# Kernel optimization log

Hardware: AMD Instinct MI355X
Metric: run time of the kernel (lower is better)

The kernel has to match this reference:

```python
import jax, jax.numpy as jnp
import numpy as np

N = 8192          # num_nodes
F_IN = 512        # num_features
D = 256           # embedding_dim
C = 40            # num_classes
E = 262144        # num_edges (avg degree 32)
ALPHA = 0.5
LN_EPS = 1e-5


def _layer_norm(x, eps=LN_EPS):
    # F.layer_norm over last dim, no affine params
    mu = jnp.mean(x, axis=-1, keepdims=True)
    var = jnp.var(x, axis=-1, keepdims=True)
    return (x - mu) * jax.lax.rsqrt(var + eps)


def setup_inputs() -> dict:
    key = jax.random.key(0)
    ks = jax.random.split(key, 16)
    s_in = 1.0 / np.sqrt(F_IN)
    s_d = 1.0 / np.sqrt(D)
    inp = {
        "X": jax.random.normal(ks[0], (N, F_IN), dtype=jnp.float32),
        "edge_row": jnp.sort(jax.random.randint(ks[1], (E,), 0, N)),
        "edge_col": jax.random.randint(ks[2], (E,), 0, N),
        "edge_weight": jax.random.uniform(ks[3], (E,), dtype=jnp.float32),
        # MLP embedding: Linear(F_IN, D)
        "W_emb": jax.random.uniform(ks[4], (F_IN, D), minval=-s_in, maxval=s_in),
        "b_emb": jax.random.uniform(ks[5], (D,), minval=-s_in, maxval=s_in),
        # attention projections: Linear(D, D) x3
        "W_q": jax.random.uniform(ks[6], (D, D), minval=-s_d, maxval=s_d),
        "b_q": jax.random.uniform(ks[7], (D,), minval=-s_d, maxval=s_d),
        "W_k": jax.random.uniform(ks[8], (D, D), minval=-s_d, maxval=s_d),
        "b_k": jax.random.uniform(ks[9], (D,), minval=-s_d, maxval=s_d),
        "W_v": jax.random.uniform(ks[10], (D, D), minval=-s_d, maxval=s_d),
        "b_v": jax.random.uniform(ks[11], (D,), minval=-s_d, maxval=s_d),
        # GNN linear: Linear(D, D)
        "W_gnn": jax.random.uniform(ks[12], (D, D), minval=-s_d, maxval=s_d),
        "b_gnn": jax.random.uniform(ks[13], (D,), minval=-s_d, maxval=s_d),
        # classifier: Linear(D, C)
        "W_cls": jax.random.uniform(ks[14], (D, C), minval=-s_d, maxval=s_d),
        "b_cls": jax.random.uniform(ks[15], (C,), minval=-s_d, maxval=s_d),
    }
    return inp


def reference(X, edge_row, edge_col, edge_weight,
              W_emb, b_emb, W_q, b_q, W_k, b_k, W_v, b_v,
              W_gnn, b_gnn, W_cls, b_cls):
    # embedding MLP
    Z0 = X @ W_emb + b_emb                      # [N, D]
    # global attention with QK layer-norm
    Q = _layer_norm(Z0 @ W_q + b_q)             # [N, D]
    K = _layer_norm(Z0 @ W_k + b_k)             # [N, D]
    V = Z0 @ W_v + b_v                          # [N, D]
    scores = Q @ K.T                            # [N, N]
    attn = jax.nn.softmax(scores, axis=-1)      # [N, N]
    Z_A = attn @ V                              # [N, D]
    # sparse GNN branch: spmm(A, linear(Z0))
    H = Z0 @ W_gnn + b_gnn                      # [N, D]
    msg = H[edge_col] * edge_weight[:, None]    # [E, D]
    gnn_out = jax.ops.segment_sum(msg, edge_row, num_segments=N)  # [N, D]
    # weighted blend + classifier
    Z_out = (1.0 - ALPHA) * Z_A + ALPHA * gnn_out
    Y_hat = Z_out @ W_cls + b_cls               # [N, C]
    return (Y_hat, attn)
```

## Files before the change

kernel.cpp:

```cpp
#include <hip/hip_runtime.h>
#include <hip/hip_bf16.h>

#define N_NODES 8192
#define F_IN    512
#define DIM     256
#define NCLS    40

typedef __attribute__((ext_vector_type(8))) short bf16x8;
typedef __attribute__((ext_vector_type(4))) float f32x4;

#define MFMA16 __builtin_amdgcn_mfma_f32_16x16x32_bf16

static __device__ __forceinline__ unsigned short f2bf(float x) {
    __hip_bfloat16 h = __float2bfloat16(x);
    return *reinterpret_cast<unsigned short*>(&h);
}
static __device__ __forceinline__ float bf2f(unsigned short u) {
    union { unsigned int u32; float f; } v; v.u32 = ((unsigned int)u) << 16;
    return v.f;
}
static __device__ __forceinline__ void gll16(const void* g, void* l) {
    __builtin_amdgcn_global_load_lds(
        (const __attribute__((address_space(1))) unsigned int*)g,
        (__attribute__((address_space(3))) unsigned int*)l, 16, 0, 0);
}

__global__ __launch_bounds__(256) void split_kernel(
    const float* __restrict__ X,
    unsigned short* __restrict__ Xh, unsigned short* __restrict__ Xl)
{
    const size_t i = ((size_t)blockIdx.x * 256 + threadIdx.x) * 4;
    float4 v = *(const float4*)&X[i];
    ushort4 h, l;
    h.x = f2bf(v.x); l.x = f2bf(v.x - bf2f(h.x));
    h.y = f2bf(v.y); l.y = f2bf(v.y - bf2f(h.y));
    h.z = f2bf(v.z); l.z = f2bf(v.z - bf2f(h.z));
    h.w = f2bf(v.w); l.w = f2bf(v.w - bf2f(h.w));
    *(ushort4*)&Xh[i] = h;
    *(ushort4*)&Xl[i] = l;
}

static __device__ __forceinline__ void wtrans_body(
    const float* __restrict__ W,
    unsigned short* __restrict__ WTh, unsigned short* __restrict__ WTl,
    int K, int N, int r0, int c0, float (*tile)[65])
{
    const int t = threadIdx.x;
    #pragma unroll
    for (int i = 0; i < 4; ++i) {
        int r = i * 16 + (t >> 4);
        int c = (t & 15) * 4;
        float4 v = *(const float4*)&W[(size_t)(r0 + r) * N + c0 + c];
        tile[r][c] = v.x; tile[r][c + 1] = v.y;
        tile[r][c + 2] = v.z; tile[r][c + 3] = v.w;
    }
    __syncthreads();
    #pragma unroll
    for (int i = 0; i < 4; ++i) {
        int c = i * 16 + (t >> 4);
        int r = (t & 15) * 4;
        ushort4 h, l;
        float x0 = tile[r][c],     x1 = tile[r + 1][c];
        float x2 = tile[r + 2][c], x3 = tile[r + 3][c];
        h.x = f2bf(x0); l.x = f2bf(x0 - bf2f(h.x));
        h.y = f2bf(x1); l.y = f2bf(x1 - bf2f(h.y));
        h.z = f2bf(x2); l.z = f2bf(x2 - bf2f(h.z));
        h.w = f2bf(x3); l.w = f2bf(x3 - bf2f(h.w));
        *(ushort4*)&WTh[(size_t)(c0 + c) * K + r0 + r] = h;
        *(ushort4*)&WTl[(size_t)(c0 + c) * K + r0 + r] = l;
    }
}

__global__ __launch_bounds__(256) void wtrans_kernel(
    const float* __restrict__ W,
    unsigned short* __restrict__ WTh, unsigned short* __restrict__ WTl,
    int K, int N)
{
    __shared__ float tile[64][65];
    wtrans_body(W, WTh, WTl, K, N, blockIdx.x * 64, blockIdx.y * 64, tile);
}

struct Wt4Args {
    const float* W[4];
    unsigned short* Th[4];
    unsigned short* Tl[4];
};

__global__ __launch_bounds__(256) void wtrans4_kernel(Wt4Args a)
{
    __shared__ float tile[64][65];
    const int z = blockIdx.z;
    wtrans_body(a.W[z], a.Th[z], a.Tl[z], DIM, DIM,
                blockIdx.x * 64, blockIdx.y * 64, tile);
}

template<int KDIM, int OUTMODE, int BM>
__device__ __forceinline__ void gemm3_body(
    const unsigned short* __restrict__ Ah_, const unsigned short* __restrict__ Al_,
    const unsigned short* __restrict__ Bh_, const unsigned short* __restrict__ Bl_,
    const float* __restrict__ bias,
    void* __restrict__ C0, void* __restrict__ C1,
    int m0, int n0,
    short (*Ah)[32], short (*Al)[32], short (*Bh)[32], short (*Bl)[32])
{
    constexpr int MFRAG = BM / 32;
    constexpr int ACH   = BM / 32;

    const int t = threadIdx.x, lane = t & 63, w = t >> 6;
    const int wm = w >> 1, wn = w & 1;
    const int fr = lane & 15, kb = lane >> 4;

    const unsigned short* asrc[ACH];
    const unsigned short* bsrc[4];
    char* adst[ACH];
    char* bdst[4];
    #pragma unroll
    for (int r = 0; r < ACH; ++r) {
        int c = r * 256 + t;
        int tens = c / (BM * 4), idx = c & (BM * 4 - 1);
        int row = idx >> 2, slot = idx & 3;
        asrc[r] = (tens ? Al_ : Ah_) + (size_t)(m0 + row) * KDIM + slot * 8;
        adst[r] = (char*)(tens ? &Al[0][0] : &Ah[0][0]) + idx * 16;
    }
    #pragma unroll
    for (int r = 0; r < 4; ++r) {
        int c = r * 256 + t;
        int tens = c >> 9, idx = c & 511;
        int row = idx >> 2, slot = idx & 3;
        bsrc[r] = (tens ? Bl_ : Bh_) + (size_t)(n0 + row) * KDIM + slot * 8;
        bdst[r] = (char*)(tens ? &Bl[0][0] : &Bh[0][0]) + idx * 16;
    }

    f32x4 acc[MFRAG][4] = {};

    for (int k0 = 0; k0 < KDIM; k0 += 32) {
        #pragma unroll
        for (int r = 0; r < ACH; ++r) { gll16(asrc[r], adst[r]); asrc[r] += 32; }
        #pragma unroll
        for (int r = 0; r < 4; ++r) { gll16(bsrc[r], bdst[r]); bsrc[r] += 32; }
        __syncthreads();

        bf16x8 ah[MFRAG], al[MFRAG], bh[4], bl[4];
        #pragma unroll
        for (int m = 0; m < MFRAG; ++m) {
            int row = wm * (BM / 2) + m * 16 + fr;
            ah[m] = *(const bf16x8*)&Ah[row][kb * 8];
            al[m] = *(const bf16x8*)&Al[row][kb * 8];
        }
        #pragma unroll
        for (int n = 0; n < 4; ++n) {
            int col = wn * 64 + n * 16 + fr;
            bh[n] = *(const bf16x8*)&Bh[col][kb * 8];
            bl[n] = *(const bf16x8*)&Bl[col][kb * 8];
        }
        #pragma unroll
        for (int m = 0; m < MFRAG; ++m)
            #pragma unroll
            for (int n = 0; n < 4; ++n) {
                acc[m][n] = MFMA16(ah[m], bh[n], acc[m][n], 0, 0, 0);
                acc[m][n] = MFMA16(ah[m], bl[n], acc[m][n], 0, 0, 0);
                acc[m][n] = MFMA16(al[m], bh[n], acc[m][n], 0, 0, 0);
            }
        __syncthreads();
    }

    #pragma unroll
    for (int m = 0; m < MFRAG; ++m)
        #pragma unroll
        for (int e = 0; e < 4; ++e) {
            const int row = m0 + wm * (BM / 2) + m * 16 + kb * 4 + e;
            #pragma unroll
            for (int n = 0; n < 4; ++n) {
                const int col = n0 + wn * 64 + n * 16 + fr;
                float v = acc[m][n][e] + bias[col];
                if (OUTMODE == 0) {
                    ((float*)C0)[(size_t)row * 256 + col] = v;
                } else if (OUTMODE == 1) {
                    ((unsigned short*)C0)[(size_t)row * 256 + col] = f2bf(v);
                } else {
                    unsigned short h = f2bf(v);
                    ((unsigned short*)C0)[(size_t)row * 256 + col] = h;
                    ((unsigned short*)C1)[(size_t)row * 256 + col] =
                        f2bf(v - bf2f(h));
                }
            }
        }
}

template<int KDIM, int OUTMODE, int BM>
__global__ __launch_bounds__(256, (BM == 64) ? 4 : 2) void mfma_gemm3_kernel(
    const unsigned short* __restrict__ Ah_, const unsigned short* __restrict__ Al_,
    const unsigned short* __restrict__ Bh_, const unsigned short* __restrict__ Bl_,
    const float* __restrict__ bias,
    void* __restrict__ C0, void* __restrict__ C1)
{
    __shared__ short Ah[BM][32], Al[BM][32], Bh[128][32], Bl[128][32];
    gemm3_body<KDIM, OUTMODE, BM>(Ah_, Al_, Bh_, Bl_, bias, C0, C1,
                                  blockIdx.y * BM, blockIdx.x * 128,
                                  Ah, Al, Bh, Bl);
}

struct Proj4Args {
    const unsigned short* Bh[4];
    const unsigned short* Bl[4];
    const float* bias[4];
    void* C[4];
};

__global__ __launch_bounds__(256, 2) void proj4_kernel(
    const unsigned short* __restrict__ Ah_, const unsigned short* __restrict__ Al_,
    Proj4Args p)
{
    __shared__ short Ah[128][32], Al[128][32], Bh[128][32], Bl[128][32];
    const int z = blockIdx.z;
    if (z < 3)
        gemm3_body<DIM, 0, 128>(Ah_, Al_, p.Bh[z], p.Bl[z], p.bias[z], p.C[z],
                                nullptr, blockIdx.y * 128, blockIdx.x * 128,
                                Ah, Al, Bh, Bl);
    else
        gemm3_body<DIM, 1, 128>(Ah_, Al_, p.Bh[z], p.Bl[z], p.bias[z], p.C[z],
                                nullptr, blockIdx.y * 128, blockIdx.x * 128,
                                Ah, Al, Bh, Bl);
}

__global__ __launch_bounds__(256) void ln_split2_kernel(
    const float* __restrict__ Qf, const float* __restrict__ Kf,
    unsigned short* __restrict__ Qh, unsigned short* __restrict__ Ql,
    unsigned short* __restrict__ Kh, unsigned short* __restrict__ Kl)
{
    const int row = blockIdx.x;
    const int t = threadIdx.x;
    const float* X = blockIdx.y ? Kf : Qf;
    unsigned short* Hi = blockIdx.y ? Kh : Qh;
    unsigned short* Lo = blockIdx.y ? Kl : Ql;

    float x = X[(size_t)row * DIM + t];

    float s1 = x, s2 = x * x;
    #pragma unroll
    for (int o = 32; o; o >>= 1) {
        s1 += __shfl_xor(s1, o);
        s2 += __shfl_xor(s2, o);
    }
    __shared__ float r1[4], r2[4];
    const int wid = t >> 6;
    if ((t & 63) == 0) { r1[wid] = s1; r2[wid] = s2; }
    __syncthreads();
    const float sum = r1[0] + r1[1] + r1[2] + r1[3];
    const float ssq = r2[0] + r2[1] + r2[2] + r2[3];
    const float mean = sum * (1.0f / DIM);
    const float var  = ssq * (1.0f / DIM) - mean * mean;
    const float y = (x - mean) * rsqrtf(var + 1e-5f);

    const unsigned short h = f2bf(y);
    Hi[(size_t)row * DIM + t] = h;
    Lo[(size_t)row * DIM + t] = f2bf(y - bf2f(h));
}

__global__ __launch_bounds__(256) void vtrans_kernel(
    const float* __restrict__ V, unsigned short* __restrict__ VT)
{
    __shared__ float tile[64][65];
    const int r0 = blockIdx.x * 64;
    const int c0 = blockIdx.y * 64;
    const int t = threadIdx.x;
    #pragma unroll
    for (int i = 0; i < 4; ++i) {
        int r = i * 16 + (t >> 4);
        int c = (t & 15) * 4;
        float4 v = *(const float4*)&V[(size_t)(r0 + r) * DIM + c0 + c];
        tile[r][c] = v.x; tile[r][c + 1] = v.y;
        tile[r][c + 2] = v.z; tile[r][c + 3] = v.w;
    }
    __syncthreads();
    #pragma unroll
    for (int i = 0; i < 4; ++i) {
        int c = i * 16 + (t >> 4);
        int r = (t & 15) * 4;
        ushort4 o;
        o.x = f2bf(tile[r][c]);     o.y = f2bf(tile[r + 1][c]);
        o.z = f2bf(tile[r + 2][c]); o.w = f2bf(tile[r + 3][c]);
        *(ushort4*)&VT[(size_t)(c0 + c) * N_NODES + r0 + r] = o;
    }
}

__global__ __launch_bounds__(256, 4) void qkt_kernel(
    const unsigned short* __restrict__ Qh, const unsigned short* __restrict__ Ql,
    const unsigned short* __restrict__ Kh, const unsigned short* __restrict__ Kl,
    unsigned short* __restrict__ Sb, float2* __restrict__ pstat)
{
    __shared__ short stage[4][128][32];
    __shared__ float2 ps[2][128];
    __shared__ float gmr[128];

    const int bid = blockIdx.x;
    const int x   = bid & 7;
    const int i   = bid >> 3;
    const int nbs = i >> 6;
    const int j   = i & 63;
    const int mb  = x * 8 + (j & 7);
    const int nb  = nbs * 8 + (j >> 3);
    const int m0 = mb * 128, n0 = nb * 128;
    const int sbbase = (nb >> 4) * 4096 + 2048 + (nb & 15) * 128;

    const int t = threadIdx.x, lane = t & 63, w = t >> 6;
    const int wm = w >> 1, wn = w & 1;
    const int fr = lane & 15, kb = lane >> 4;

    const unsigned short* qsrc[2][2];
    const unsigned short* ksrc[2][2];
    char* qdst[2][2];
    char* kdst[2][2];
    #pragma unroll
    for (int r = 0; r < 2; ++r) {
        int c = r * 256 + t;
        int row = c >> 2, slot = c & 3;
        size_t ga = (size_t)(m0 + row) * DIM + slot * 8;
        size_t gb = (size_t)(n0 + row) * DIM + slot * 8;
        qsrc[r][0] = Qh + ga; qsrc[r][1] = Ql + ga;
        ksrc[r][0] = Kh + gb; ksrc[r][1] = Kl + gb;
        qdst[r][0] = (char*)&stage[0][0][0] + c * 16;
        qdst[r][1] = (char*)&stage[1][0][0] + c * 16;
        kdst[r][0] = (char*)&stage[2][0][0] + c * 16;
        kdst[r][1] = (char*)&stage[3][0][0] + c * 16;
    }

    f32x4 acc[4][4] = {};

    for (int k0 = 0; k0 < DIM; k0 += 32) {
        #pragma unroll
        for (int r = 0; r < 2; ++r) {
            gll16(qsrc[r][0], qdst[r][0]); qsrc[r][0] += 32;
            gll16(qsrc[r][1], qdst[r][1]); qsrc[r][1] += 32;
            gll16(ksrc[r][0], kdst[r][0]); ksrc[r][0] += 32;
            gll16(ksrc[r][1], kdst[r][1]); ksrc[r][1] += 32;
        }
        __syncthreads();

        bf16x8 ah[4], al[4], bh[4], bl[4];
        #pragma unroll
        for (int m = 0; m < 4; ++m) {
            int row = wm * 64 + m * 16 + fr;
            ah[m] = *(const bf16x8*)&stage[0][row][kb * 8];
            al[m] = *(const bf16x8*)&stage[1][row][kb * 8];
        }
        #pragma unroll
        for (int n = 0; n < 4; ++n) {
            int col = wn * 64 + n * 16 + fr;
            bh[n] = *(const bf16x8*)&stage[2][col][kb * 8];
            bl[n] = *(const bf16x8*)&stage[3][col][kb * 8];
        }
        #pragma unroll
        for (int m = 0; m < 4; ++m)
            #pragma unroll
            for (int n = 0; n < 4; ++n) {
                acc[m][n] = MFMA16(ah[m], bh[n], acc[m][n], 0, 0, 0);
                acc[m][n] = MFMA16(ah[m], bl[n], acc[m][n], 0, 0, 0);
                acc[m][n] = MFMA16(al[m], bh[n], acc[m][n], 0, 0, 0);
            }
        __syncthreads();
    }

    #pragma unroll
    for (int m = 0; m < 4; ++m)
        #pragma unroll
        for (int e = 0; e < 4; ++e) {
            float mx = acc[m][0][e];
            #pragma unroll
            for (int n = 1; n < 4; ++n) mx = fmaxf(mx, acc[m][n][e]);
            #pragma unroll
            for (int o = 1; o < 16; o <<= 1) mx = fmaxf(mx, __shfl_xor(mx, o));
            if (fr == 0) ps[wn][wm * 64 + m * 16 + kb * 4 + e].x = mx;
        }
    __syncthreads();
    if (t < 128) gmr[t] = fmaxf(ps[0][t].x, ps[1][t].x);
    __syncthreads();

    unsigned short* tile = (unsigned short*)&stage[0][0][0];
    #pragma unroll
    for (int m = 0; m < 4; ++m)
        #pragma unroll
        for (int e = 0; e < 4; ++e) {
            const int rl = wm * 64 + m * 16 + kb * 4 + e;
            const float g = gmr[rl];
            const int key = kb << 1;
            float se = 0.f;
            #pragma unroll
            for (int n = 0; n < 4; ++n) {
                float ev = __expf(acc[m][n][e] - g);
                se += ev;
                const int col = wn * 64 + n * 16 + fr;
                tile[rl * 128 + (((col >> 3) ^ key) << 3) + (col & 7)] =
                    f2bf(ev);
            }
            #pragma unroll
            for (int o = 1; o < 16; o <<= 1) se += __shfl_xor(se, o);
            if (fr == 0) ps[wn][rl].y = se;
        }
    __syncthreads();
    if (t < 128)
        pstat[(size_t)(m0 + t) * 64 + nb] =
            make_float2(gmr[t], ps[0][t].y + ps[1][t].y);

    #pragma unroll
    for (int p = 0; p < 8; ++p) {
        int c = p * 256 + t;
        int r = c >> 4, sl = c & 15;
        int slx = sl ^ (((r >> 2) & 3) << 1);
        *(int4*)&Sb[(size_t)(m0 + r) * 16384 + sbbase + sl * 8] =
            *(const int4*)((const char*)tile + (r * 16 + slx) * 16);
    }
}

__global__ __launch_bounds__(512, 2) void av_mfma_kernel(
    const unsigned short* __restrict__ Sb, const float2* __restrict__ pstat,
    const unsigned short* __restrict__ VT, float* __restrict__ attn,
    float* __restrict__ P0, float* __restrict__ P1,
    float* __restrict__ P2, float* __restrict__ P3)
{
    __shared__ unsigned short As[2][64][128];
    __shared__ float facsT[16][64];

    const int bid = blockIdx.x;
    const int x = bid & 7, i = bid >> 3;
    const int ks = i >> 4;
    const int rb = (i & 15) * 8 + x;
    const int r0 = rb * 64, kbase = ks * 2048, cb0 = ks * 16;
    const int t = threadIdx.x;
    const bool producer = (t < 256);
    const int tp = t & 255;
    const int lane = tp & 63, w = tp >> 6;
    const int fr = lane & 15, kb = lane >> 4;

    {
        const int row = t >> 3;
        const int sub = t & 7;
        const float2* pp = pstat + (size_t)(r0 + row) * 64 + sub * 8;
        float m = -3.0e38f, s = 0.f;
        #pragma unroll
        for (int jj = 0; jj < 8; ++jj) {
            float2 v = pp[jj];
            float nm = fmaxf(m, v.x);
            s = s * __expf(m - nm) + v.y * __expf(v.x - nm);
            m = nm;
        }
        #pragma unroll
        for (int o = 1; o < 8; o <<= 1) {
            float om = __shfl_xor(m, o);
            float os = __shfl_xor(s, o);
            float nm = fmaxf(m, om);
            s = s * __expf(m - nm) + os * __expf(om - nm);
            m = nm;
        }
        const float inv = 1.0f / s;
        #pragma unroll
        for (int jj = 0; jj < 2; ++jj) {
            int cb = sub * 2 + jj;
            float2 v = pstat[(size_t)(r0 + row) * 64 + cb0 + cb];
            facsT[cb][row] = __expf(v.x - m) * inv;
        }
    }

    const unsigned short* vb[4];
    #pragma unroll
    for (int n = 0; n < 4; ++n)
        vb[n] = VT + (size_t)(w * 64 + n * 16 + fr) * N_NODES + kbase + kb * 8;

    const unsigned short* ssrc[4];
    char* sdst[4];
    #pragma unroll
    for (int p = 0; p < 4; ++p) {
        int c = p * 256 + tp;
        int rr = c >> 4, sl = c & 15;
        int slp = sl ^ (rr & 7);
        ssrc[p] = Sb + (size_t)(r0 + rr) * 16384 + ks * 4096 + 2048 + slp * 8;
        sdst[p] = (char*)&As[0][0][0] + c * 16;
    }

    #define STAGE(BUF_) do {                                                  \
        _Pragma("unroll")                                                     \
        for (int p = 0; p < 4; ++p) {                                         \
            gll16(ssrc[p], sdst[p] + (BUF_) * 16384);                         \
            ssrc[p] += 128;                                                   \
        } } while (0)

    f32x4 acc[4][4] = {};
    const f32x4 z4 = {0.f, 0.f, 0.f, 0.f};

    if (producer) STAGE(0);
    __syncthreads();

    for (int s = 0; s < 16; ++s) {
        const int b = s & 1;
        const char* abase = (const char*)&As[b][0][0];

        if (producer) {
            if (s + 1 < 16) STAGE(b ^ 1);

            bf16x8 bb[4][4];
            #pragma unroll
            for (int ksl = 0; ksl < 4; ++ksl)
                #pragma unroll
                for (int n = 0; n < 4; ++n)
                    bb[ksl][n] = *(const bf16x8*)(vb[n] + s * 128 + ksl * 32);

            #pragma unroll
            for (int m = 0; m < 4; ++m) {
                f32x4 sacc[4];
                {
                    bf16x8 a = *(const bf16x8*)(abase + (m * 16 + fr) * 256 +
                                                ((kb ^ (fr & 7)) * 16));
                    #pragma unroll
                    for (int n = 0; n < 4; ++n)
                        sacc[n] = MFMA16(a, bb[0][n], z4, 0, 0, 0);
                }
                #pragma unroll
                for (int ksl = 1; ksl < 4; ++ksl) {
                    bf16x8 a = *(const bf16x8*)(abase + (m * 16 + fr) * 256 +
                                                (((ksl * 4 + kb) ^ (fr & 7)) * 16));
                    #pragma unroll
                    for (int n = 0; n < 4; ++n)
                        sacc[n] = MFMA16(a, bb[ksl][n], sacc[n], 0, 0, 0);
                }
                f32x4 fac = *(const f32x4*)&facsT[s][m * 16 + kb * 4];
                #pragma unroll
                for (int n = 0; n < 4; ++n)
                    acc[m][n] += fac * sacc[n];
            }
        } else {
            #pragma unroll
            for (int p = 0; p < 4; ++p) {
                int ci = p * 256 + tp;
                int rr = ci >> 4, g = ci & 15;
                const float fac = facsT[s][rr];
                int4 v = *(const int4*)(abase + (rr * 16 + (g ^ (rr & 7))) * 16);
                float* dst = attn + (size_t)(r0 + rr) * N_NODES +
                             kbase + s * 128 + g * 8;
                float4 o0, o1;
                o0.x = bf2f((unsigned short)(v.x & 0xffff)) * fac;
                o0.y = bf2f((unsigned short)((unsigned)v.x >> 16)) * fac;
                o0.z = bf2f((unsigned short)(v.y & 0xffff)) * fac;
                o0.w = bf2f((unsigned short)((unsigned)v.y >> 16)) * fac;
                o1.x = bf2f((unsigned short)(v.z & 0xffff)) * fac;
                o1.y = bf2f((unsigned short)((unsigned)v.z >> 16)) * fac;
                o1.z = bf2f((unsigned short)(v.w & 0xffff)) * fac;
                o1.w = bf2f((unsigned short)((unsigned)v.w >> 16)) * fac;
                *(float4*)dst       = o0;
                *(float4*)(dst + 4) = o1;
            }
        }
        __syncthreads();
    }
    #undef STAGE

    if (producer) {
        float* P = (ks == 0) ? P0 : (ks == 1) ? P1 : (ks == 2) ? P2 : P3;
        #pragma unroll
        for (int m = 0; m < 4; ++m)
            #pragma unroll
            for (int e = 0; e < 4; ++e) {
                int row = r0 + m * 16 + kb * 4 + e;
                #pragma unroll
                for (int n = 0; n < 4; ++n)
                    P[(size_t)row * DIM + w * 64 + n * 16 + fr] = acc[m][n][e];
            }
    }
}

__global__ __launch_bounds__(256) void spmm_kernel(
    const unsigned short* __restrict__ Hb, const int* __restrict__ erow,
    const int* __restrict__ ecol, const float* __restrict__ ew,
    float* __restrict__ out, int E)
{
    const int node = blockIdx.x * 4 + (threadIdx.x >> 6);
    const int lane = threadIdx.x & 63;

    int lo = 0, hi = E;
    while (lo < hi) { int mid = (lo + hi) >> 1; if (erow[mid] < node) lo = mid + 1; else hi = mid; }
    const int beg = lo;
    hi = E;
    while (lo < hi) { int mid = (lo + hi) >> 1; if (erow[mid] < node + 1) lo = mid + 1; else hi = mid; }
    const int end = lo;

    float4 acc = make_float4(0.f, 0.f, 0.f, 0.f);
    for (int e = beg; e < end; ++e) {
        const int col = ecol[e];
        const float wgt = ew[e];
        ushort4 h = *(const ushort4*)&Hb[(size_t)col * DIM + lane * 4];
        acc.x += wgt * bf2f(h.x);
        acc.y += wgt * bf2f(h.y);
        acc.z += wgt * bf2f(h.z);
        acc.w += wgt * bf2f(h.w);
    }
    *(float4*)&out[(size_t)node * DIM + lane * 4] = acc;
}

__global__ __launch_bounds__(256) void blend_cls_kernel(
    const float* __restrict__ p0, const float* __restrict__ p1,
    const float* __restrict__ p2, const float* __restrict__ p3,
    const float* __restrict__ gnn,
    const float* __restrict__ Wc, const float* __restrict__ bc,
    float* __restrict__ Y)
{
    const int row = blockIdx.x;
    const int t = threadIdx.x;
    __shared__ float z[DIM];
    __shared__ float part[4][NCLS];

    const size_t i = (size_t)row * DIM + t;
    z[t] = 0.5f * (p0[i] + p1[i] + p2[i] + p3[i] + gnn[i]);
    __syncthreads();

    if (t < 160) {
        const int c = t % NCLS, q = t / NCLS;
        float acc = 0.0f;
        #pragma unroll 4
        for (int d = q * 64; d < q * 64 + 64; ++d)
            acc += z[d] * Wc[d * NCLS + c];
        part[q][c] = acc;
    }
    __syncthreads();
    if (t < NCLS)
        Y[(size_t)row * NCLS + t] =
            part[0][t] + part[1][t] + part[2][t] + part[3][t] + bc[t];
}

extern "C" void kernel_launch(void* const* d_in, const int* in_sizes, int n_in,
                              void* d_out, int out_size, void* d_ws, size_t ws_size,
                              hipStream_t stream)
{
    const float* X     = (const float*)d_in[0];
    const int*   erow  = (const int*)d_in[1];
    const int*   ecol  = (const int*)d_in[2];
    const float* ew    = (const float*)d_in[3];
    const float* W_emb = (const float*)d_in[4];
    const float* b_emb = (const float*)d_in[5];
    const float* W_q   = (const float*)d_in[6];
    const float* b_q   = (const float*)d_in[7];
    const float* W_k   = (const float*)d_in[8];
    const float* b_k   = (const float*)d_in[9];
    const float* W_v   = (const float*)d_in[10];
    const float* b_v   = (const float*)d_in[11];
    const float* W_g   = (const float*)d_in[12];
    const float* b_g   = (const float*)d_in[13];
    const float* W_c   = (const float*)d_in[14];
    const float* b_c   = (const float*)d_in[15];
    const int E = in_sizes[1];

    float* Y    = (float*)d_out;
    float* Sc   = Y + (size_t)N_NODES * NCLS;
    unsigned short* Sb = (unsigned short*)Sc;

    const size_t ND = (size_t)N_NODES * DIM;
    float* R0 = (float*)d_ws;
    float* R1 = R0 + ND;
    float* R2 = R1 + ND;
    float* R3 = R2 + ND;
    float* R4 = R3 + ND;
    float* R5 = R4 + ND;
    float* R6 = R5 + ND;

    unsigned short* Xh = (unsigned short*)R0;
    unsigned short* Xl = (unsigned short*)R1;
    unsigned short* Wt = (unsigned short*)R2;
    unsigned short* WembTh = Wt;
    unsigned short* WembTl = Wt + 256 * 512;
    unsigned short* WqTh = WembTl + 256 * 512;
    unsigned short* WqTl = WqTh + 256 * 256;
    unsigned short* WkTh = WqTl + 256 * 256;
    unsigned short* WkTl = WkTh + 256 * 256;
    unsigned short* WvTh = WkTl + 256 * 256;
    unsigned short* WvTl = WvTh + 256 * 256;
    unsigned short* WgTh = WvTl + 256 * 256;
    unsigned short* WgTl = WgTh + 256 * 256;
    unsigned short* Z0h = (unsigned short*)R3;
    unsigned short* Z0l = Z0h + ND;
    float* Qf = R4;
    float* Kf = R5;
    float* Vf = R6;
    unsigned short* Hb = (unsigned short*)R0;
    unsigned short* Qh = (unsigned short*)R1;
    unsigned short* Ql = Qh + ND;
    unsigned short* Kh = (unsigned short*)R2;
    unsigned short* Kl = Kh + ND;
    unsigned short* VT = (unsigned short*)(R0 + ND / 2);
    float2* pstat = (float2*)R4;
    float* P0 = R6;
    float* P1 = R3;
    float* P2 = R5;
    float* P3 = R1;
    float* GNN = R2;

    split_kernel<<<(N_NODES * F_IN) / 1024, 256, 0, stream>>>(X, Xh, Xl);

    wtrans_kernel<<<dim3(F_IN / 64, DIM / 64), 256, 0, stream>>>(
        W_emb, WembTh, WembTl, F_IN, DIM);
    Wt4Args wa;
    wa.W[0] = W_q; wa.Th[0] = WqTh; wa.Tl[0] = WqTl;
    wa.W[1] = W_k; wa.Th[1] = WkTh; wa.Tl[1] = WkTl;
    wa.W[2] = W_v; wa.Th[2] = WvTh; wa.Tl[2] = WvTl;
    wa.W[3] = W_g; wa.Th[3] = WgTh; wa.Tl[3] = WgTl;
    wtrans4_kernel<<<dim3(DIM / 64, DIM / 64, 4), 256, 0, stream>>>(wa);

    mfma_gemm3_kernel<F_IN, 2, 64><<<dim3(2, N_NODES / 64), 256, 0, stream>>>(
        Xh, Xl, WembTh, WembTl, b_emb, Z0h, Z0l);

    Proj4Args pa;
    pa.Bh[0] = WqTh; pa.Bl[0] = WqTl; pa.bias[0] = b_q; pa.C[0] = Qf;
    pa.Bh[1] = WkTh; pa.Bl[1] = WkTl; pa.bias[1] = b_k; pa.C[1] = Kf;
    pa.Bh[2] = WvTh; pa.Bl[2] = WvTl; pa.bias[2] = b_v; pa.C[2] = Vf;
    pa.Bh[3] = WgTh; pa.Bl[3] = WgTl; pa.bias[3] = b_g; pa.C[3] = Hb;
    proj4_kernel<<<dim3(2, N_NODES / 128, 4), 256, 0, stream>>>(Z0h, Z0l, pa);

    ln_split2_kernel<<<dim3(N_NODES, 2), 256, 0, stream>>>(
        Qf, Kf, Qh, Ql, Kh, Kl);

    vtrans_kernel<<<dim3(N_NODES / 64, DIM / 64), 256, 0, stream>>>(Vf, VT);

    qkt_kernel<<<4096, 256, 0, stream>>>(Qh, Ql, Kh, Kl, Sb, pstat);

    av_mfma_kernel<<<512, 512, 0, stream>>>(
        Sb, pstat, VT, Sc, P0, P1, P2, P3);

    spmm_kernel<<<N_NODES / 4, 256, 0, stream>>>(Hb, erow, ecol, ew, GNN, E);

    blend_cls_kernel<<<N_NODES, 256, 0, stream>>>(
        P0, P1, P2, P3, GNN, W_c, b_c, Y);
}
```

Measured before the change: 402.8 us.

## Widen QK^T block tile to 128x256 with 8 waves sharing Q tile

Each block of the QK^T kernel now covers 256 key columns instead of 128, using 512 threads (8 waves), so the Q hi/lo tile staged in LDS is reused across twice as many columns and fewer blocks are launched. Row max is reduced across four column-waves, and the exp/bf16 write-out of scores is done in two halves through a shared staging tile, each emitting its own per-128-column pstat entry. This reduces redundant Q loads and per-block overhead, at the cost of extra barriers in the epilogue and lower block count/occupancy flexibility.

```diff
diff --git a/kernel.cpp b/kernel.cpp
--- a/kernel.cpp
+++ b/kernel.cpp
@@ -284,57 +284,53 @@
     }
 }
 
-__global__ __launch_bounds__(256, 4) void qkt_kernel(
-    const unsigned short* __restrict__ Qh, const unsigned short* __restrict__ Ql,
-    const unsigned short* __restrict__ Kh, const unsigned short* __restrict__ Kl,
+__global__ __launch_bounds__(512, 2) void qkt_kernel(
+    const unsigned short* __restrict__ Qh_, const unsigned short* __restrict__ Ql_,
+    const unsigned short* __restrict__ Kh_, const unsigned short* __restrict__ Kl_,
     unsigned short* __restrict__ Sb, float2* __restrict__ pstat)
 {
-    __shared__ short stage[4][128][32];
-    __shared__ float2 ps[2][128];
+    __shared__ short stage[3][256][32];
+    __shared__ float2 ps[4][128];
     __shared__ float gmr[128];
 
     const int bid = blockIdx.x;
     const int x   = bid & 7;
     const int i   = bid >> 3;
-    const int nbs = i >> 6;
+    const int nps = i >> 6;
     const int j   = i & 63;
     const int mb  = x * 8 + (j & 7);
-    const int nb  = nbs * 8 + (j >> 3);
-    const int m0 = mb * 128, n0 = nb * 128;
-    const int sbbase = (nb >> 4) * 4096 + 2048 + (nb & 15) * 128;
+    const int nbp = nps * 8 + (j >> 3);
+    const int m0 = mb * 128, n0 = nbp * 256;
+    const int nb0 = nbp * 2;
 
     const int t = threadIdx.x, lane = t & 63, w = t >> 6;
-    const int wm = w >> 1, wn = w & 1;
+    const int wm = w >> 2, wn = w & 3;
     const int fr = lane & 15, kb = lane >> 4;
 
-    const unsigned short* qsrc[2][2];
-    const unsigned short* ksrc[2][2];
-    char* qdst[2][2];
-    char* kdst[2][2];
-    #pragma unroll
-    for (int r = 0; r < 2; ++r) {
-        int c = r * 256 + t;
-        int row = c >> 2, slot = c & 3;
-        size_t ga = (size_t)(m0 + row) * DIM + slot * 8;
-        size_t gb = (size_t)(n0 + row) * DIM + slot * 8;
-        qsrc[r][0] = Qh + ga; qsrc[r][1] = Ql + ga;
-        ksrc[r][0] = Kh + gb; ksrc[r][1] = Kl + gb;
-        qdst[r][0] = (char*)&stage[0][0][0] + c * 16;
-        qdst[r][1] = (char*)&stage[1][0][0] + c * 16;
-        kdst[r][0] = (char*)&stage[2][0][0] + c * 16;
-        kdst[r][1] = (char*)&stage[3][0][0] + c * 16;
+    const unsigned short* src[6];
+    char* dst[6];
+    #pragma unroll
+    for (int r = 0; r < 6; ++r) {
+        int c = r * 512 + t;
+        if (c < 1024) {
+            int tens = c >> 9, idx = c & 511;
+            int row = idx >> 2, slot = idx & 3;
+            src[r] = (tens ? Ql_ : Qh_) + (size_t)(m0 + row) * DIM + slot * 8;
+            dst[r] = (char*)&stage[0][0][0] + c * 16;
+        } else {
+            int cb = c - 1024;
+            int tens = cb >> 10, idx = cb & 1023;
+            int row = idx >> 2, slot = idx & 3;
+            src[r] = (tens ? Kl_ : Kh_) + (size_t)(n0 + row) * DIM + slot * 8;
+            dst[r] = (char*)&stage[1][0][0] + cb * 16;
+        }
     }
 
     f32x4 acc[4][4] = {};
 
     for (int k0 = 0; k0 < DIM; k0 += 32) {
         #pragma unroll
-        for (int r = 0; r < 2; ++r) {
-            gll16(qsrc[r][0], qdst[r][0]); qsrc[r][0] += 32;
-            gll16(qsrc[r][1], qdst[r][1]); qsrc[r][1] += 32;
-            gll16(ksrc[r][0], kdst[r][0]); ksrc[r][0] += 32;
-            gll16(ksrc[r][1], kdst[r][1]); ksrc[r][1] += 32;
-        }
+        for (int r = 0; r < 6; ++r) { gll16(src[r], dst[r]); src[r] += 32; }
         __syncthreads();
 
         bf16x8 ah[4], al[4], bh[4], bl[4];
@@ -342,13 +338,13 @@
         for (int m = 0; m < 4; ++m) {
             int row = wm * 64 + m * 16 + fr;
             ah[m] = *(const bf16x8*)&stage[0][row][kb * 8];
-            al[m] = *(const bf16x8*)&stage[1][row][kb * 8];
+            al[m] = *(const bf16x8*)&stage[0][128 + row][kb * 8];
         }
         #pragma unroll
         for (int n = 0; n < 4; ++n) {
             int col = wn * 64 + n * 16 + fr;
-            bh[n] = *(const bf16x8*)&stage[2][col][kb * 8];
-            bl[n] = *(const bf16x8*)&stage[3][col][kb * 8];
+            bh[n] = *(const bf16x8*)&stage[1][col][kb * 8];
+            bl[n] = *(const bf16x8*)&stage[2][col][kb * 8];
         }
         #pragma unroll
         for (int m = 0; m < 4; ++m)
@@ -373,42 +369,52 @@
             if (fr == 0) ps[wn][wm * 64 + m * 16 + kb * 4 + e].x = mx;
         }
     __syncthreads();
-    if (t < 128) gmr[t] = fmaxf(ps[0][t].x, ps[1][t].x);
+    if (t < 128)
+        gmr[t] = fmaxf(fmaxf(ps[0][t].x, ps[1][t].x),
+                       fmaxf(ps[2][t].x, ps[3][t].x));
     __syncthreads();
 
-    unsigned short* tile = (unsigned short*)&stage[0][0][0];
-    #pragma unroll
-    for (int m = 0; m < 4; ++m)
-        #pragma unroll
-        for (int e = 0; e < 4; ++e) {
-            const int rl = wm * 64 + m * 16 + kb * 4 + e;
-            const float g = gmr[rl];
-            const int key = kb << 1;
-            float se = 0.f;
-            #pragma unroll
-            for (int n = 0; n < 4; ++n) {
-                float ev = __expf(acc[m][n][e] - g);
-                se += ev;
-                const int col = wn * 64 + n * 16 + fr;
-                tile[rl * 128 + (((col >> 3) ^ key) << 3) + (col & 7)] =
-                    f2bf(ev);
-            }
-            #pragma unroll
-            for (int o = 1; o < 16; o <<= 1) se += __shfl_xor(se, o);
-            if (fr == 0) ps[wn][rl].y = se;
-        }
-    __syncthreads();
-    if (t < 128)
-        pstat[(size_t)(m0 + t) * 64 + nb] =
-            make_float2(gmr[t], ps[0][t].y + ps[1][t].y);
-
-    #pragma unroll
-    for (int p = 0; p < 8; ++p) {
-        int c = p * 256 + t;
-        int r = c >> 4, sl = c & 15;
-        int slx = sl ^ (((r >> 2) & 3) << 1);
-        *(int4*)&Sb[(size_t)(m0 + r) * 16384 + sbbase + sl * 8] =
-            *(const int4*)((const char*)tile + (r * 16 + slx) * 16);
+    unsigned short* tile = (unsigned short*)&stage[1][0][0];
+    #pragma unroll
+    for (int hf = 0; hf < 2; ++hf) {
+        if ((wn >> 1) == hf) {
+            #pragma unroll
+            for (int m = 0; m < 4; ++m)
+                #pragma unroll
+                for (int e = 0; e < 4; ++e) {
+                    const int rl = wm * 64 + m * 16 + kb * 4 + e;
+                    const float g = gmr[rl];
+                    const int key = kb << 1;
+                    float se = 0.f;
+                    #pragma unroll
+                    for (int n = 0; n < 4; ++n) {
+                        float ev = __expf(acc[m][n][e] - g);
+                        se += ev;
+                        const int col = (wn & 1) * 64 + n * 16 + fr;
+                        tile[rl * 128 + (((col >> 3) ^ key) << 3) + (col & 7)]
+                            = f2bf(ev);
+                    }
+                    #pragma unroll
+                    for (int o = 1; o < 16; o <<= 1) se += __shfl_xor(se, o);
+                    if (fr == 0) ps[wn][rl].y = se;
+                }
+        }
+        __syncthreads();
+
+        const int nb = nb0 + hf;
+        const int sbb = (nb >> 4) * 4096 + 2048 + (nb & 15) * 128;
+        #pragma unroll
+        for (int p = 0; p < 4; ++p) {
+            int c = p * 512 + t;
+            int r = c >> 4, sl = c & 15;
+            int slx = sl ^ (((r >> 2) & 3) << 1);
+            *(int4*)&Sb[(size_t)(m0 + r) * 16384 + sbb + sl * 8] =
+                *(const int4*)((const char*)tile + (r * 16 + slx) * 16);
+        }
+        if (t < 128)
+            pstat[(size_t)(m0 + t) * 64 + nb] =
+                make_float2(gmr[t], ps[2 * hf][t].y + ps[2 * hf + 1][t].y);
+        __syncthreads();
     }
 }
 
@@ -717,7 +723,7 @@
 
     vtrans_kernel<<<dim3(N_NODES / 64, DIM / 64), 256, 0, stream>>>(Vf, VT);
 
-    qkt_kernel<<<4096, 256, 0, stream>>>(Qh, Ql, Kh, Kl, Sb, pstat);
+    qkt_kernel<<<2048, 512, 0, stream>>>(Qh, Ql, Kh, Kl, Sb, pstat);
 
     av_mfma_kernel<<<512, 512, 0, stream>>>(
         Sb, pstat, VT, Sc, P0, P1, P2, P3);
```

Measured after the change: 453.1 us. 1.13x slower.
